# Kernel optimization log

Measured on AMD Instinct MI355X. Metric: run time of the kernel, lower is better.

## Reference

```python
import jax, jax.numpy as jnp
import numpy as np

N_NODES = 50000
N_EDGES = 800000
FEAT = 64
N_LAYERS = 3


def setup_inputs() -> dict:
    key = jax.random.key(0)
    ks = jax.random.split(key, 6)
    x = jax.random.normal(ks[0], (N_NODES, FEAT), dtype=jnp.float32)
    edge_index = jax.random.randint(ks[1], (2, N_EDGES), 0, N_NODES, dtype=jnp.int64)
    s = 1.0 / np.sqrt(2 * FEAT)
    W1 = jax.random.uniform(ks[2], (N_LAYERS, 2 * FEAT, FEAT), jnp.float32, -s, s)
    b1 = jax.random.uniform(ks[3], (N_LAYERS, FEAT), jnp.float32, -s, s)
    s2 = 1.0 / np.sqrt(FEAT)
    W2 = jax.random.uniform(ks[4], (N_LAYERS, FEAT, FEAT), jnp.float32, -s2, s2)
    b2 = jax.random.uniform(ks[5], (N_LAYERS, FEAT), jnp.float32, -s2, s2)
    return {"x": x, "edge_index": edge_index, "W1": W1, "b1": b1, "W2": W2, "b2": b2}


def _edgeconv(x, src, dst, W1, b1, W2, b2):
    # PyG EdgeConv: message = mlp([x_i, x_j - x_i]), aggr = max over incoming edges
    xi = x[dst]                                  # [E, F] target features
    xj = x[src]                                  # [E, F] source features
    m = jnp.concatenate([xi, xj - xi], axis=-1)  # [E, 2F]
    h = jax.nn.relu(m @ W1 + b1)                 # [E, F]
    h = h @ W2 + b2                              # [E, F]
    out = jax.ops.segment_max(h, dst, num_segments=x.shape[0])
    # isolated nodes: -inf -> 0 (matches torch_scatter max fill)
    return jnp.where(jnp.isfinite(out), out, 0.0)


def reference(x, edge_index, W1, b1, W2, b2):
    src, dst = edge_index[0], edge_index[1]
    for l in range(N_LAYERS):
        x = _edgeconv(x, src, dst, W1[l], b1[l], W2[l], b2[l])
        x = jax.nn.relu(x)
    return x
```

## Files before the change

kernel.cpp:

```cpp
#include <hip/hip_runtime.h>

#define NN 50000
#define NE 800000
#define F  64
#define NBKT 196
#define CHUNK (NE / 256)

typedef __attribute__((ext_vector_type(8))) short bf16x8;
typedef __attribute__((ext_vector_type(4))) float f32x4;

#define WS_FLAG   0u
#define WS_WCTH   256u
#define WS_WCTL   49408u
#define WS_W2TH   98560u
#define WS_W2TL   123136u
#define WS_SEDGE  147712u
#define WS_U      3347712u
#define WS_V      16147712u
#define WS_BHT    (WS_U + 0u)
#define WS_BOT    (WS_U + 200960u)
#define WS_CSUM   (WS_U + 401920u)
#define WS_BASE   (WS_U + 402944u)
#define WS_TMP    (WS_V + 0u)

__device__ __forceinline__ float relu_f(float a) { return a > 0.f ? a : 0.f; }

__device__ __forceinline__ void pack4(float f0, float f1, float f2, float f3,
                                      unsigned& hw0, unsigned& hw1,
                                      unsigned& lw0, unsigned& lw1) {
    unsigned u0 = __float_as_uint(f0), u1 = __float_as_uint(f1);
    unsigned u2 = __float_as_uint(f2), u3 = __float_as_uint(f3);
    unsigned h0 = u0 & 0xffff0000u, h1 = u1 & 0xffff0000u;
    unsigned h2 = u2 & 0xffff0000u, h3 = u3 & 0xffff0000u;
    float l0 = f0 - __uint_as_float(h0), l1 = f1 - __uint_as_float(h1);
    float l2 = f2 - __uint_as_float(h2), l3 = f3 - __uint_as_float(h3);
    hw0 = h1 | (h0 >> 16);
    hw1 = h3 | (h2 >> 16);
    lw0 = (__float_as_uint(l1) & 0xffff0000u) | (__float_as_uint(l0) >> 16);
    lw1 = (__float_as_uint(l3) & 0xffff0000u) | (__float_as_uint(l2) >> 16);
}

__device__ __forceinline__ void glds16(const float* g, void* l) {
    __builtin_amdgcn_global_load_lds(
        (const __attribute__((address_space(1))) unsigned*)g,
        (__attribute__((address_space(3))) unsigned*)l, 16, 0, 0);
}

__device__ __forceinline__ int permJ(int j) { return (j >= 4 && j < 12) ? (j ^ 12) : j; }

__global__ void detect_kernel(const int* __restrict__ idx, int* __restrict__ flag) {
    int t = blockIdx.x * blockDim.x + threadIdx.x;
    if (idx[2 * t + 1] != 0) atomicOr(flag, 1);
}

__global__ void prep_kernel(const float* __restrict__ W1, const float* __restrict__ W2,
                            unsigned short* __restrict__ WCTH, unsigned short* __restrict__ WCTL,
                            unsigned short* __restrict__ W2TH, unsigned short* __restrict__ W2TL) {
    int i = blockIdx.x * blockDim.x + threadIdx.x;
    int l = i >> 12;
    int r = i & 4095;
    int k = r >> 6;
    int j = r & 63;
    float wa = W1[l * 8192 + k * 64 + j];
    float wb = W1[l * 8192 + 4096 + k * 64 + j];
    float a = wa - wb;
    unsigned ua = __float_as_uint(a), ahi = ua & 0xffff0000u;
    float alo = a - __uint_as_float(ahi);
    WCTH[l * 8192 + j * 64 + k] = (unsigned short)(ahi >> 16);
    WCTL[l * 8192 + j * 64 + k] = (unsigned short)(__float_as_uint(alo) >> 16);
    unsigned ub = __float_as_uint(wb), bhi = ub & 0xffff0000u;
    float blo = wb - __uint_as_float(bhi);
    WCTH[l * 8192 + (64 + j) * 64 + k] = (unsigned short)(bhi >> 16);
    WCTL[l * 8192 + (64 + j) * 64 + k] = (unsigned short)(__float_as_uint(blo) >> 16);
    float w = W2[l * 4096 + k * 64 + j];
    unsigned uw = __float_as_uint(w), whi = uw & 0xffff0000u;
    float wlo = w - __uint_as_float(whi);
    W2TH[l * 4096 + j * 64 + k] = (unsigned short)(whi >> 16);
    W2TL[l * 4096 + j * 64 + k] = (unsigned short)(__float_as_uint(wlo) >> 16);
}

__global__ __launch_bounds__(256, 2) void gemm_mfma(
    const float* __restrict__ xin,
    const unsigned short* __restrict__ WCTH, const unsigned short* __restrict__ WCTL,
    const float* __restrict__ b1,
    float* __restrict__ U, float* __restrict__ V) {
    __shared__ char smem[65536];
    int lane = threadIdx.x & 63;
    int wib  = threadIdx.x >> 6;
    char* base = smem + wib * 16384;
    char* Hhi = base;
    char* Hlo = base + 8192;
    int l15 = lane & 15, l4 = lane >> 4;

    int wid = blockIdx.x * 4 + wib;
    int b = wid >> 1;
    int half = wid & 1;

    bf16x8 Bh[2][4], Bl[2][4];
#pragma unroll
    for (int kt = 0; kt < 2; ++kt)
#pragma unroll
        for (int nt = 0; nt < 4; ++nt) {
            int off = (half * 64 + nt * 16 + l15) * 64 + kt * 32 + l4 * 8;
            Bh[kt][nt] = *(const bf16x8*)(WCTH + off);
            Bl[kt][nt] = *(const bf16x8*)(WCTL + off);
        }

    int jj = lane & 15;
    int rsub = lane >> 4;
#pragma unroll
    for (int i = 0; i < 16; ++i) {
        int r = 4 * i + rsub;
        int node = b * 64 + r;
        int cnode = node < NN ? node : NN - 1;
        float4 xv = *(const float4*)(xin + (size_t)cnode * F + 4 * jj);
        unsigned hw0, hw1, lw0, lw1;
        pack4(xv.x, xv.y, xv.z, xv.w, hw0, hw1, lw0, lw1);
        int g = jj >> 1;
        int byt = r * 128 + ((g ^ (r & 7)) << 4) + (jj & 1) * 8;
        *(uint2*)(Hhi + byt) = make_uint2(hw0, hw1);
        *(uint2*)(Hlo + byt) = make_uint2(lw0, lw1);
    }

    f32x4 acc[4][4];
#pragma unroll
    for (int mt = 0; mt < 4; ++mt)
#pragma unroll
        for (int nt = 0; nt < 4; ++nt)
            acc[mt][nt] = (f32x4){0.f, 0.f, 0.f, 0.f};
#pragma unroll
    for (int mt = 0; mt < 4; ++mt) {
        int arow = mt * 16 + l15;
        int abase = arow * 128;
        int am = arow & 7;
        bf16x8 Ah0 = *(const bf16x8*)(Hhi + abase + (((0 + l4) ^ am) << 4));
        bf16x8 Ah1 = *(const bf16x8*)(Hhi + abase + (((4 + l4) ^ am) << 4));
        bf16x8 Al0 = *(const bf16x8*)(Hlo + abase + (((0 + l4) ^ am) << 4));
        bf16x8 Al1 = *(const bf16x8*)(Hlo + abase + (((4 + l4) ^ am) << 4));
#pragma unroll
        for (int nt = 0; nt < 4; ++nt) {
            f32x4 a = acc[mt][nt];
            a = __builtin_amdgcn_mfma_f32_16x16x32_bf16(Ah0, Bh[0][nt], a, 0, 0, 0);
            a = __builtin_amdgcn_mfma_f32_16x16x32_bf16(Ah1, Bh[1][nt], a, 0, 0, 0);
            a = __builtin_amdgcn_mfma_f32_16x16x32_bf16(Al0, Bh[0][nt], a, 0, 0, 0);
            a = __builtin_amdgcn_mfma_f32_16x16x32_bf16(Al1, Bh[1][nt], a, 0, 0, 0);
            a = __builtin_amdgcn_mfma_f32_16x16x32_bf16(Ah0, Bl[0][nt], a, 0, 0, 0);
            a = __builtin_amdgcn_mfma_f32_16x16x32_bf16(Ah1, Bl[1][nt], a, 0, 0, 0);
            acc[mt][nt] = a;
        }
    }

    float bc[4];
#pragma unroll
    for (int nt = 0; nt < 4; ++nt)
        bc[nt] = (half == 0) ? b1[nt * 16 + l15] : 0.f;
    float* outp = (half == 0) ? U : V;
#pragma unroll
    for (int mt = 0; mt < 4; ++mt)
#pragma unroll
        for (int nt = 0; nt < 4; ++nt) {
            int col = nt * 16 + l15;
#pragma unroll
            for (int r = 0; r < 4; ++r) {
                int row = b * 64 + mt * 16 + l4 * 4 + r;
                if (row < NN) outp[(size_t)row * F + col] = acc[mt][nt][r] + bc[nt];
            }
        }
}

__global__ __launch_bounds__(256) void histA_kernel(const int* __restrict__ idx,
                                                    const int* __restrict__ flag,
                                                    int* __restrict__ bhistT) {
    __shared__ int h[NBKT];
    int tid = threadIdx.x, blk = blockIdx.x;
    if (tid < NBKT) h[tid] = 0;
    __syncthreads();
    int fl = *flag;
    int start = blk * CHUNK;
    for (int i = tid; i < CHUNK; i += 256) {
        int e = start + i;
        int dst = fl ? idx[NE + e] : idx[2 * NE + 2 * e];
        atomicAdd(&h[dst >> 8], 1);
    }
    __syncthreads();
    if (tid < NBKT) bhistT[tid * 256 + blk] = h[tid];
}

__global__ __launch_bounds__(256) void scanCols_kernel(const int* __restrict__ bhistT,
                                                       int* __restrict__ boffT,
                                                       int* __restrict__ csum) {
    __shared__ int buf[256];
    int t = threadIdx.x, b = blockIdx.x;
    int v = bhistT[b * 256 + t];
    buf[t] = v;
    __syncthreads();
    for (int d = 1; d < 256; d <<= 1) {
        int add = (t >= d) ? buf[t - d] : 0;
        __syncthreads();
        buf[t] += add;
        __syncthreads();
    }
    boffT[b * 256 + t] = buf[t] - v;
    if (t == 255) csum[b] = buf[255];
}

__global__ __launch_bounds__(256) void scanBase_kernel(const int* __restrict__ csum,
                                                       int* __restrict__ base) {
    __shared__ int buf[256];
    int t = threadIdx.x;
    int v = (t < NBKT) ? csum[t] : 0;
    buf[t] = v;
    __syncthreads();
    for (int d = 1; d < 256; d <<= 1) {
        int add = (t >= d) ? buf[t - d] : 0;
        __syncthreads();
        buf[t] += add;
        __syncthreads();
    }
    if (t < NBKT) base[t] = buf[t] - v;
}

__global__ __launch_bounds__(256) void scatterA2_kernel(const int* __restrict__ idx,
                                                        const int* __restrict__ flag,
                                                        const int* __restrict__ boffT,
                                                        const int* __restrict__ base,
                                                        unsigned* __restrict__ tmp) {
    __shared__ int loc[NBKT];
    __shared__ int bb[NBKT];
    int tid = threadIdx.x, blk = blockIdx.x;
    if (tid < NBKT) { loc[tid] = 0; bb[tid] = base[tid] + boffT[tid * 256 + blk]; }
    __syncthreads();
    int fl = *flag;
    int start = blk * CHUNK;
    for (int i = tid; i < CHUNK; i += 256) {
        int e = start + i;
        int src, dst;
        if (fl) { src = idx[e];     dst = idx[NE + e]; }
        else    { src = idx[2 * e]; dst = idx[2 * NE + 2 * e]; }
        int bkt = dst >> 8;
        int my = atomicAdd(&loc[bkt], 1);
        tmp[bb[bkt] + my] = ((unsigned)dst << 16) | (unsigned)src;
    }
}

__global__ __launch_bounds__(256) void sortC_kernel(const unsigned* __restrict__ tmp,
                                                    const int* __restrict__ base,
                                                    const int* __restrict__ csum,
                                                    unsigned* __restrict__ sedge) {
    __shared__ int cnt[256];
    __shared__ int pos[256];
    int b = blockIdx.x, t = threadIdx.x;
    int start = base[b], n = csum[b];
    cnt[t] = 0;
    __syncthreads();
    for (int i = t; i < n; i += 256)
        atomicAdd(&cnt[(tmp[start + i] >> 16) & 255], 1);
    __syncthreads();
    int v = cnt[t];
    pos[t] = v;
    __syncthreads();
    for (int d = 1; d < 256; d <<= 1) {
        int add = (t >= d) ? pos[t - d] : 0;
        __syncthreads();
        pos[t] += add;
        __syncthreads();
    }
    int excl = pos[t] - v;
    __syncthreads();
    pos[t] = excl;
    __syncthreads();
    for (int i = t; i < n; i += 256) {
        unsigned w = tmp[start + i];
        int p = atomicAdd(&pos[(w >> 16) & 255], 1);
        sedge[start + p] = w;
    }
}

#define WSTR 18944
__global__ __launch_bounds__(128, 2) void edge_kernel(
    const unsigned* __restrict__ sedge,
    const float* __restrict__ U, const float* __restrict__ V,
    const unsigned short* __restrict__ W2TH, const unsigned short* __restrict__ W2TL,
    const float* __restrict__ b2, float* __restrict__ out) {
    __shared__ char smem[2 * WSTR];
    int lane = threadIdx.x & 63;
    int wib  = threadIdx.x >> 6;
    char* R = smem + wib * WSTR;
    float* seg = (float*)(R + 16384);
    unsigned* ebuf = (unsigned*)(R + 18432);
    int l15 = lane & 15, l4 = lane >> 4;
    int jj = lane & 15, rsub = lane >> 4;

    float bias = b2[lane];

    bf16x8 Bh[2][4], Bl[2][4];
#pragma unroll
    for (int kt = 0; kt < 2; ++kt)
#pragma unroll
        for (int nt = 0; nt < 4; ++nt) {
            int off = (nt * 16 + l15) * 64 + kt * 32 + l4 * 8;
            Bh[kt][nt] = *(const bf16x8*)(W2TH + off);
            Bl[kt][nt] = *(const bf16x8*)(W2TL + off);
        }

    int bid = blockIdx.x;
    int swz = (bid & 7) * 128 + (bid >> 3);
    int wid = swz * 2 + wib;
    const int NB = NE / 64;
    int bstart = (int)(((long long)wid * NB) >> 11);
    int bend   = (int)(((long long)(wid + 1) * NB) >> 11);
    if (bstart >= bend) return;

    float run = -3.402823e38f;
    int   segdst = -1;
    bool  firstflush = true;

    unsigned pe = sedge[bstart * 64 + lane];
    ebuf[(bstart & 1) * 64 + lane] = pe;
    {
        const unsigned* ebn = ebuf + (bstart & 1) * 64;
#pragma unroll
        for (int k = 0; k < 16; ++k) {
            int pk = permJ(k);
            unsigned ew = ebn[4 * pk + l4];
            int sr = (int)(ew & 0xffffu);
            glds16(V + (size_t)sr * F + 4 * jj, R + k * 1024);
        }
    }

    for (int b = bstart; b < bend; ++b) {
        int par = b & 1;
        const unsigned* eb = ebuf + par * 64;

        unsigned pe_n = 0;
        if (b + 1 < bend) pe_n = sedge[(b + 1) * 64 + lane];

        asm volatile("s_waitcnt vmcnt(0)" ::: "memory");
        __builtin_amdgcn_sched_barrier(0);

        int dst = (int)(pe >> 16);

#pragma unroll
        for (int h = 0; h < 2; ++h) {
            float4 vvr[8], uu[8];
#pragma unroll
            for (int q = 0; q < 8; ++q) {
                int j = 8 * h + q;
                int k = permJ(j);
                vvr[q] = *(const float4*)(R + k * 1024 + rsub * 256 + jj * 16);
            }
#pragma unroll
            for (int q = 0; q < 8; ++q) {
                int row = 32 * h + 4 * q + rsub;
                unsigned ew = eb[row];
                int dr = (int)(ew >> 16);
                uu[q] = *(const float4*)(U + (size_t)dr * F + 4 * jj);
            }
#pragma unroll
            for (int q = 0; q < 8; ++q) {
                int r = 32 * h + 4 * q + rsub;
                float4 ua = uu[q], va = vvr[q];
                unsigned hw0, hw1, lw0, lw1;
                pack4(relu_f(ua.x + va.x), relu_f(ua.y + va.y),
                      relu_f(ua.z + va.z), relu_f(ua.w + va.w), hw0, hw1, lw0, lw1);
                int g = jj >> 1;
                int byt = r * 128 + ((g ^ (r & 7)) << 4) + (jj & 1) * 8;
                *(uint2*)(R + byt) = make_uint2(hw0, hw1);
                *(uint2*)(R + 8192 + byt) = make_uint2(lw0, lw1);
            }
        }

        int pdst = __shfl_up(dst, 1, 64);
        bool leader = (lane == 0) || (pdst != dst);
        unsigned long long lead = __ballot(leader);

        f32x4 acc[4][4];
#pragma unroll
        for (int mt = 0; mt < 4; ++mt)
#pragma unroll
            for (int nt = 0; nt < 4; ++nt)
                acc[mt][nt] = (f32x4){0.f, 0.f, 0.f, 0.f};
#pragma unroll
        for (int mt = 0; mt < 4; ++mt) {
            int arow = mt * 16 + l15;
            int abase = arow * 128;
            int am = arow & 7;
            bf16x8 Ah0 = *(const bf16x8*)(R + abase + (((0 + l4) ^ am) << 4));
            bf16x8 Ah1 = *(const bf16x8*)(R + abase + (((4 + l4) ^ am) << 4));
            bf16x8 Al0 = *(const bf16x8*)(R + 8192 + abase + (((0 + l4) ^ am) << 4));
            bf16x8 Al1 = *(const bf16x8*)(R + 8192 + abase + (((4 + l4) ^ am) << 4));
#pragma unroll
            for (int nt = 0; nt < 4; ++nt) {
                f32x4 a = acc[mt][nt];
                a = __builtin_amdgcn_mfma_f32_16x16x32_bf16(Ah0, Bh[0][nt], a, 0, 0, 0);
                a = __builtin_amdgcn_mfma_f32_16x16x32_bf16(Ah1, Bh[1][nt], a, 0, 0, 0);
                a = __builtin_amdgcn_mfma_f32_16x16x32_bf16(Al0, Bh[0][nt], a, 0, 0, 0);
                a = __builtin_amdgcn_mfma_f32_16x16x32_bf16(Al1, Bh[1][nt], a, 0, 0, 0);
                a = __builtin_amdgcn_mfma_f32_16x16x32_bf16(Ah0, Bl[0][nt], a, 0, 0, 0);
                a = __builtin_amdgcn_mfma_f32_16x16x32_bf16(Ah1, Bl[1][nt], a, 0, 0, 0);
                acc[mt][nt] = a;
            }
        }

        __builtin_amdgcn_sched_barrier(0);
        if (b + 1 < bend) {
            ebuf[(par ^ 1) * 64 + lane] = pe_n;
            const unsigned* ebn = ebuf + (par ^ 1) * 64;
#pragma unroll
            for (int k = 0; k < 16; ++k) {
                int pk = permJ(k);
                unsigned ew = ebn[4 * pk + l4];
                int sr = (int)(ew & 0xffffu);
                glds16(V + (size_t)sr * F + 4 * jj, R + k * 1024);
            }
        }

        int used = __popcll(lead);
        int sid[4][4];
#pragma unroll
        for (int mt = 0; mt < 4; ++mt)
#pragma unroll
            for (int r = 0; r < 4; ++r) {
                int row = mt * 16 + l4 * 4 + r;
                sid[mt][r] = __popcll(lead & ((2ull << row) - 1ull)) - 1;
            }

        unsigned long long mwalk = lead;
        for (int sb = 0; sb < used; sb += 8) {
            int ns = used - sb; if (ns > 8) ns = 8;
            for (int s = 0; s < ns; ++s) seg[s * 64 + lane] = -3.402823e38f;
#pragma unroll
            for (int mt = 0; mt < 4; ++mt)
#pragma unroll
                for (int nt = 0; nt < 4; ++nt)
#pragma unroll
                    for (int r = 0; r < 4; ++r) {
                        int t = sid[mt][r] - sb;
                        if ((unsigned)t < 8u)
                            (void)__hip_atomic_fetch_max(
                                &seg[t * 64 + nt * 16 + l15], acc[mt][nt][r],
                                __ATOMIC_RELAXED, __HIP_MEMORY_SCOPE_WAVEFRONT);
                    }
            for (int s = 0; s < ns; ++s) {
                int rb = __ffsll((long long)mwalk) - 1; mwalk &= mwalk - 1ull;
                int dsts = __shfl(dst, rb, 64);
                float val = seg[s * 64 + lane];
                if (dsts != segdst) {
                    if (segdst >= 0) {
                        float v = fmaxf(run + bias, 0.f);
                        if (firstflush) {
                            if (v > 0.f)
                                atomicMax((int*)(out + (size_t)segdst * F + lane),
                                          __float_as_int(v));
                            firstflush = false;
                        } else {
                            out[(size_t)segdst * F + lane] = v;
                        }
                    }
                    segdst = dsts; run = val;
                } else run = fmaxf(run, val);
            }
        }

        pe = pe_n;
    }
    if (segdst >= 0) {
        float val = fmaxf(run + bias, 0.f);
        if (val > 0.f)
            atomicMax((int*)(out + (size_t)segdst * F + lane), __float_as_int(val));
    }
}

extern "C" void kernel_launch(void* const* d_in, const int* in_sizes, int n_in,
                              void* d_out, int out_size, void* d_ws, size_t ws_size,
                              hipStream_t stream) {
    const float* x  = (const float*)d_in[0];
    const int*   ei = (const int*)d_in[1];
    const float* W1 = (const float*)d_in[2];
    const float* b1 = (const float*)d_in[3];
    const float* W2 = (const float*)d_in[4];
    const float* b2 = (const float*)d_in[5];
    float* out = (float*)d_out;

    char* ws = (char*)d_ws;
    int*            flag   = (int*)(ws + WS_FLAG);
    unsigned short* WCTH   = (unsigned short*)(ws + WS_WCTH);
    unsigned short* WCTL   = (unsigned short*)(ws + WS_WCTL);
    unsigned short* W2TH   = (unsigned short*)(ws + WS_W2TH);
    unsigned short* W2TL   = (unsigned short*)(ws + WS_W2TL);
    unsigned*       sedge  = (unsigned*)(ws + WS_SEDGE);
    float*          Ubuf   = (float*)(ws + WS_U);
    float*          Vbuf   = (float*)(ws + WS_V);
    int*            bhistT = (int*)(ws + WS_BHT);
    int*            boffT  = (int*)(ws + WS_BOT);
    int*            csum   = (int*)(ws + WS_CSUM);
    int*            baseb  = (int*)(ws + WS_BASE);
    unsigned*       tmp    = (unsigned*)(ws + WS_TMP);

    hipMemsetAsync(flag, 0, 4, stream);
    detect_kernel<<<16, 256, 0, stream>>>(ei, flag);
    prep_kernel<<<48, 256, 0, stream>>>(W1, W2, WCTH, WCTL, W2TH, W2TL);
    histA_kernel<<<256, 256, 0, stream>>>(ei, flag, bhistT);
    scanCols_kernel<<<NBKT, 256, 0, stream>>>(bhistT, boffT, csum);
    scanBase_kernel<<<1, 256, 0, stream>>>(csum, baseb);
    scatterA2_kernel<<<256, 256, 0, stream>>>(ei, flag, boffT, baseb, tmp);
    sortC_kernel<<<NBKT, 256, 0, stream>>>(tmp, baseb, csum, sedge);

    const float* xin = x;
    for (int l = 0; l < 3; ++l) {
        gemm_mfma<<<391, 256, 0, stream>>>(xin, WCTH + l * 8192, WCTL + l * 8192,
                                           b1 + l * 64, Ubuf, Vbuf);
        hipMemsetAsync(out, 0, (size_t)NN * F * sizeof(float), stream);
        edge_kernel<<<1024, 128, 0, stream>>>(sedge, Ubuf, Vbuf,
                                              W2TH + l * 4096, W2TL + l * 4096,
                                              b2 + l * 64, out);
        xin = out;
    }
}
```

Baseline: 286.7 us.

## Halve edge batch to 32 rows and drop async V prefetch for higher occupancy

The edge kernel now processes 32 edges per wave iteration instead of 64, which shrinks per-wave LDS and accumulator registers and raises launch bounds to four blocks per SM. It removes the global_load_lds double-buffered prefetch of source features and loads U and V rows directly into registers. W2 fragments are reloaded per iteration from global memory through scalar-pinned pointers instead of being held in registers. The aim is to hide gather latency with more resident waves rather than explicit prefetch. In exchange it gives up software pipelining, pays for repeated W2 loads, and runs twice as many loop iterations, each with its own segment-flush overhead.

```diff
diff --git a/kernel.cpp b/kernel.cpp
--- a/kernel.cpp
+++ b/kernel.cpp
@@ -39,14 +39,6 @@
     lw0 = (__float_as_uint(l1) & 0xffff0000u) | (__float_as_uint(l0) >> 16);
     lw1 = (__float_as_uint(l3) & 0xffff0000u) | (__float_as_uint(l2) >> 16);
 }
-
-__device__ __forceinline__ void glds16(const float* g, void* l) {
-    __builtin_amdgcn_global_load_lds(
-        (const __attribute__((address_space(1))) unsigned*)g,
-        (__attribute__((address_space(3))) unsigned*)l, 16, 0, 0);
-}
-
-__device__ __forceinline__ int permJ(int j) { return (j >= 4 && j < 12) ? (j ^ 12) : j; }
 
 __global__ void detect_kernel(const int* __restrict__ idx, int* __restrict__ flag) {
     int t = blockIdx.x * blockDim.x + threadIdx.x;
@@ -276,8 +268,9 @@
     }
 }
 
-#define WSTR 18944
-__global__ __launch_bounds__(128, 2) void edge_kernel(
+#define EB 32
+#define WSTR 9984
+__global__ __launch_bounds__(128, 4) void edge_kernel(
     const unsigned* __restrict__ sedge,
     const float* __restrict__ U, const float* __restrict__ V,
     const unsigned short* __restrict__ W2TH, const unsigned short* __restrict__ W2TL,
@@ -286,27 +279,19 @@
     int lane = threadIdx.x & 63;
     int wib  = threadIdx.x >> 6;
     char* R = smem + wib * WSTR;
-    float* seg = (float*)(R + 16384);
-    unsigned* ebuf = (unsigned*)(R + 18432);
+    char* Hhi = R;
+    char* Hlo = R + 4096;
+    float* seg = (float*)(R + 8192);
+    unsigned* ebuf = (unsigned*)(R + 9728);
     int l15 = lane & 15, l4 = lane >> 4;
     int jj = lane & 15, rsub = lane >> 4;
 
     float bias = b2[lane];
-
-    bf16x8 Bh[2][4], Bl[2][4];
-#pragma unroll
-    for (int kt = 0; kt < 2; ++kt)
-#pragma unroll
-        for (int nt = 0; nt < 4; ++nt) {
-            int off = (nt * 16 + l15) * 64 + kt * 32 + l4 * 8;
-            Bh[kt][nt] = *(const bf16x8*)(W2TH + off);
-            Bl[kt][nt] = *(const bf16x8*)(W2TL + off);
-        }
 
     int bid = blockIdx.x;
     int swz = (bid & 7) * 128 + (bid >> 3);
     int wid = swz * 2 + wib;
-    const int NB = NE / 64;
+    const int NB = NE / EB;
     int bstart = (int)(((long long)wid * NB) >> 11);
     int bend   = (int)(((long long)(wid + 1) * NB) >> 11);
     if (bstart >= bend) return;
@@ -315,134 +300,112 @@
     int   segdst = -1;
     bool  firstflush = true;
 
-    unsigned pe = sedge[bstart * 64 + lane];
-    ebuf[(bstart & 1) * 64 + lane] = pe;
-    {
-        const unsigned* ebn = ebuf + (bstart & 1) * 64;
-#pragma unroll
-        for (int k = 0; k < 16; ++k) {
-            int pk = permJ(k);
-            unsigned ew = ebn[4 * pk + l4];
-            int sr = (int)(ew & 0xffffu);
-            glds16(V + (size_t)sr * F + 4 * jj, R + k * 1024);
-        }
-    }
-
     for (int b = bstart; b < bend; ++b) {
-        int par = b & 1;
-        const unsigned* eb = ebuf + par * 64;
-
-        unsigned pe_n = 0;
-        if (b + 1 < bend) pe_n = sedge[(b + 1) * 64 + lane];
-
-        asm volatile("s_waitcnt vmcnt(0)" ::: "memory");
-        __builtin_amdgcn_sched_barrier(0);
-
+        unsigned pe = sedge[b * EB + (lane & 31)];
         int dst = (int)(pe >> 16);
+        ebuf[lane & 31] = pe;
+
+        unsigned pr[8];
+#pragma unroll
+        for (int i = 0; i < 8; ++i) pr[i] = ebuf[4 * i + rsub];
 
 #pragma unroll
         for (int h = 0; h < 2; ++h) {
-            float4 vvr[8], uu[8];
-#pragma unroll
-            for (int q = 0; q < 8; ++q) {
-                int j = 8 * h + q;
-                int k = permJ(j);
-                vvr[q] = *(const float4*)(R + k * 1024 + rsub * 256 + jj * 16);
-            }
-#pragma unroll
-            for (int q = 0; q < 8; ++q) {
-                int row = 32 * h + 4 * q + rsub;
-                unsigned ew = eb[row];
-                int dr = (int)(ew >> 16);
-                uu[q] = *(const float4*)(U + (size_t)dr * F + 4 * jj);
-            }
-#pragma unroll
-            for (int q = 0; q < 8; ++q) {
-                int r = 32 * h + 4 * q + rsub;
-                float4 ua = uu[q], va = vvr[q];
+            float4 uu[4], vv[4];
+#pragma unroll
+            for (int q = 0; q < 4; ++q) {
+                unsigned p = pr[4 * h + q];
+                uu[q] = *(const float4*)(U + (size_t)(p >> 16) * F + 4 * jj);
+                vv[q] = *(const float4*)(V + (size_t)(p & 0xffffu) * F + 4 * jj);
+            }
+#pragma unroll
+            for (int q = 0; q < 4; ++q) {
+                int r = 4 * (4 * h + q) + rsub;
+                float4 ua = uu[q], va = vv[q];
                 unsigned hw0, hw1, lw0, lw1;
                 pack4(relu_f(ua.x + va.x), relu_f(ua.y + va.y),
                       relu_f(ua.z + va.z), relu_f(ua.w + va.w), hw0, hw1, lw0, lw1);
                 int g = jj >> 1;
                 int byt = r * 128 + ((g ^ (r & 7)) << 4) + (jj & 1) * 8;
-                *(uint2*)(R + byt) = make_uint2(hw0, hw1);
-                *(uint2*)(R + 8192 + byt) = make_uint2(lw0, lw1);
+                *(uint2*)(Hhi + byt) = make_uint2(hw0, hw1);
+                *(uint2*)(Hlo + byt) = make_uint2(lw0, lw1);
             }
         }
 
         int pdst = __shfl_up(dst, 1, 64);
-        bool leader = (lane == 0) || (pdst != dst);
-        unsigned long long lead = __ballot(leader);
-
-        f32x4 acc[4][4];
-#pragma unroll
-        for (int mt = 0; mt < 4; ++mt)
-#pragma unroll
-            for (int nt = 0; nt < 4; ++nt)
-                acc[mt][nt] = (f32x4){0.f, 0.f, 0.f, 0.f};
-#pragma unroll
-        for (int mt = 0; mt < 4; ++mt) {
+        bool leader = ((lane & 31) == 0) || (pdst != dst);
+        unsigned lead = (unsigned)__ballot(leader);
+
+        bf16x8 A[2][4];
+#pragma unroll
+        for (int mt = 0; mt < 2; ++mt) {
             int arow = mt * 16 + l15;
             int abase = arow * 128;
             int am = arow & 7;
-            bf16x8 Ah0 = *(const bf16x8*)(R + abase + (((0 + l4) ^ am) << 4));
-            bf16x8 Ah1 = *(const bf16x8*)(R + abase + (((4 + l4) ^ am) << 4));
-            bf16x8 Al0 = *(const bf16x8*)(R + 8192 + abase + (((0 + l4) ^ am) << 4));
-            bf16x8 Al1 = *(const bf16x8*)(R + 8192 + abase + (((4 + l4) ^ am) << 4));
-#pragma unroll
-            for (int nt = 0; nt < 4; ++nt) {
+            A[mt][0] = *(const bf16x8*)(Hhi + abase + (((0 + l4) ^ am) << 4));
+            A[mt][1] = *(const bf16x8*)(Hhi + abase + (((4 + l4) ^ am) << 4));
+            A[mt][2] = *(const bf16x8*)(Hlo + abase + (((0 + l4) ^ am) << 4));
+            A[mt][3] = *(const bf16x8*)(Hlo + abase + (((4 + l4) ^ am) << 4));
+        }
+
+        const unsigned short* w2h = W2TH;
+        const unsigned short* w2l = W2TL;
+        asm volatile("" : "+s"(w2h), "+s"(w2l));
+
+        f32x4 acc[2][4];
+#pragma unroll
+        for (int mt = 0; mt < 2; ++mt)
+#pragma unroll
+            for (int nt = 0; nt < 4; ++nt)
+                acc[mt][nt] = (f32x4){0.f, 0.f, 0.f, 0.f};
+#pragma unroll
+        for (int nt = 0; nt < 4; ++nt) {
+            int boff = (nt * 16 + l15) * 64 + l4 * 8;
+            bf16x8 Bh0 = *(const bf16x8*)(w2h + boff);
+            bf16x8 Bh1 = *(const bf16x8*)(w2h + boff + 32);
+            bf16x8 Bl0 = *(const bf16x8*)(w2l + boff);
+            bf16x8 Bl1 = *(const bf16x8*)(w2l + boff + 32);
+#pragma unroll
+            for (int mt = 0; mt < 2; ++mt) {
                 f32x4 a = acc[mt][nt];
-                a = __builtin_amdgcn_mfma_f32_16x16x32_bf16(Ah0, Bh[0][nt], a, 0, 0, 0);
-                a = __builtin_amdgcn_mfma_f32_16x16x32_bf16(Ah1, Bh[1][nt], a, 0, 0, 0);
-                a = __builtin_amdgcn_mfma_f32_16x16x32_bf16(Al0, Bh[0][nt], a, 0, 0, 0);
-                a = __builtin_amdgcn_mfma_f32_16x16x32_bf16(Al1, Bh[1][nt], a, 0, 0, 0);
-                a = __builtin_amdgcn_mfma_f32_16x16x32_bf16(Ah0, Bl[0][nt], a, 0, 0, 0);
-                a = __builtin_amdgcn_mfma_f32_16x16x32_bf16(Ah1, Bl[1][nt], a, 0, 0, 0);
+                a = __builtin_amdgcn_mfma_f32_16x16x32_bf16(A[mt][0], Bh0, a, 0, 0, 0);
+                a = __builtin_amdgcn_mfma_f32_16x16x32_bf16(A[mt][1], Bh1, a, 0, 0, 0);
+                a = __builtin_amdgcn_mfma_f32_16x16x32_bf16(A[mt][2], Bh0, a, 0, 0, 0);
+                a = __builtin_amdgcn_mfma_f32_16x16x32_bf16(A[mt][3], Bh1, a, 0, 0, 0);
+                a = __builtin_amdgcn_mfma_f32_16x16x32_bf16(A[mt][0], Bl0, a, 0, 0, 0);
+                a = __builtin_amdgcn_mfma_f32_16x16x32_bf16(A[mt][1], Bl1, a, 0, 0, 0);
                 acc[mt][nt] = a;
             }
         }
 
-        __builtin_amdgcn_sched_barrier(0);
-        if (b + 1 < bend) {
-            ebuf[(par ^ 1) * 64 + lane] = pe_n;
-            const unsigned* ebn = ebuf + (par ^ 1) * 64;
-#pragma unroll
-            for (int k = 0; k < 16; ++k) {
-                int pk = permJ(k);
-                unsigned ew = ebn[4 * pk + l4];
-                int sr = (int)(ew & 0xffffu);
-                glds16(V + (size_t)sr * F + 4 * jj, R + k * 1024);
-            }
-        }
-
-        int used = __popcll(lead);
-        int sid[4][4];
-#pragma unroll
-        for (int mt = 0; mt < 4; ++mt)
+        int used = __popc(lead);
+        int sid[2][4];
+#pragma unroll
+        for (int mt = 0; mt < 2; ++mt)
 #pragma unroll
             for (int r = 0; r < 4; ++r) {
                 int row = mt * 16 + l4 * 4 + r;
-                sid[mt][r] = __popcll(lead & ((2ull << row) - 1ull)) - 1;
-            }
-
-        unsigned long long mwalk = lead;
-        for (int sb = 0; sb < used; sb += 8) {
-            int ns = used - sb; if (ns > 8) ns = 8;
+                sid[mt][r] = __popc(lead & ((2u << row) - 1u)) - 1;
+            }
+
+        unsigned mwalk = lead;
+        for (int sb = 0; sb < used; sb += 6) {
+            int ns = used - sb; if (ns > 6) ns = 6;
             for (int s = 0; s < ns; ++s) seg[s * 64 + lane] = -3.402823e38f;
 #pragma unroll
-            for (int mt = 0; mt < 4; ++mt)
+            for (int mt = 0; mt < 2; ++mt)
 #pragma unroll
                 for (int nt = 0; nt < 4; ++nt)
 #pragma unroll
                     for (int r = 0; r < 4; ++r) {
                         int t = sid[mt][r] - sb;
-                        if ((unsigned)t < 8u)
+                        if ((unsigned)t < 6u)
                             (void)__hip_atomic_fetch_max(
                                 &seg[t * 64 + nt * 16 + l15], acc[mt][nt][r],
                                 __ATOMIC_RELAXED, __HIP_MEMORY_SCOPE_WAVEFRONT);
                     }
             for (int s = 0; s < ns; ++s) {
-                int rb = __ffsll((long long)mwalk) - 1; mwalk &= mwalk - 1ull;
+                int rb = __ffs(mwalk) - 1; mwalk &= mwalk - 1u;
                 int dsts = __shfl(dst, rb, 64);
                 float val = seg[s * 64 + lane];
                 if (dsts != segdst) {
@@ -461,8 +424,6 @@
                 } else run = fmaxf(run, val);
             }
         }
-
-        pe = pe_n;
     }
     if (segdst >= 0) {
         float val = fmaxf(run + bias, 0.f);
```

After: 362.9 us. +26.6%, slower.
